# Performance work log

Hardware: AMD Instinct MI355X
Metric: run time of the kernel (lower is better)

The kernel has to match this reference:

```python
import jax, jax.numpy as jnp
import numpy as np

T = 5
EPS = 1e-05


def setup_inputs() -> dict:
    key = jax.random.key(0)
    X = jax.random.normal(key, (64, 512, 32, 32), dtype=jnp.float32)
    return {"X": X}


def reference(X):
    # IterNorm (training branch): whiten channels via Newton-Schulz inverse sqrt.
    N, C, H, W = X.shape
    x = jnp.transpose(X, (1, 0, 2, 3)).reshape(C, -1)  # [d, m], d=C, m=N*H*W
    d, m = x.shape
    mean = jnp.mean(x, axis=-1, keepdims=True)
    xc = x - mean
    I = jnp.eye(d, dtype=X.dtype)
    # Sigma = eps*I + (1/m) xc xc^T  (addmm(eps, I, 1/m, xc, xc^T))
    Sigma = EPS * I + (xc @ xc.T) / m
    rTr = 1.0 / jnp.trace(Sigma)          # (Sigma * I).sum().reciprocal()
    Sigma_N = Sigma * rTr
    P = I
    for _ in range(T):
        # P_{k+1} = 1.5*P_k - 0.5 * P_k^3 @ Sigma_N
        P = 1.5 * P - 0.5 * (P @ P @ P) @ Sigma_N
    wm = P * jnp.sqrt(rTr)                # whitening matrix ~ Sigma^{-1/2}
    xn = wm @ xc                          # [d, m]
    Xn = jnp.transpose(xn.reshape(C, N, H, W), (1, 0, 2, 3))
    return Xn
```

## Files before the change

kernel.cpp:

```cpp
#include <hip/hip_runtime.h>
#include <math.h>

#define Nn   64
#define Cc   512
#define HWs  1024
#define CHW  (Cc * HWs)
#define Mm   (Nn * HWs)
#define EPSC 1e-5f

typedef unsigned int   u32;
typedef unsigned short u16;
typedef __attribute__((ext_vector_type(8))) short  short8;
typedef __attribute__((ext_vector_type(4))) float  floatx4;

__device__ __forceinline__ u16 f2bf(float f) {
    u32 u = __float_as_uint(f);
    u += 0x7fff + ((u >> 16) & 1);
    return (u16)(u >> 16);
}
__device__ __forceinline__ float bf2f(u16 h) {
    return __uint_as_float(((u32)h) << 16);
}

__device__ __forceinline__ void gld_lds16(const u16* g, u16* l) {
    __builtin_amdgcn_global_load_lds(
        (const __attribute__((address_space(1))) u32*)g,
        (__attribute__((address_space(3))) u32*)l, 16, 0, 0);
}

__global__ __launch_bounds__(256) void convert_transpose(const float* __restrict__ X,
                                                         u16* __restrict__ Xbf,
                                                         u16* __restrict__ Xt,
                                                         float* __restrict__ meanP) {
    const int hT = blockIdx.x;
    const int h0 = hT << 6;
    const int c0 = blockIdx.y << 6;
    const int n  = blockIdx.z;
    const int t  = threadIdx.x;
    __shared__ u16   T[64][65];
    __shared__ float red[64][17];

    const float* Xn  = X   + (size_t)n * CHW;
    u16*         Xbn = Xbf + (size_t)n * CHW;
    u16*         Xtn = Xt  + (size_t)n * CHW;

    const int cl = t >> 4;
    const int h4 = (t & 15) << 2;
#pragma unroll
    for (int i = 0; i < 4; ++i) {
        const int c = cl + (i << 4);
        float4 v = *(const float4*)&Xn[(size_t)(c0 + c) * HWs + h0 + h4];
        red[c][t & 15] = v.x + v.y + v.z + v.w;
        u16 b0 = f2bf(v.x), b1 = f2bf(v.y), b2 = f2bf(v.z), b3 = f2bf(v.w);
        *(ushort4*)&Xbn[(size_t)(c0 + c) * HWs + h0 + h4] = make_ushort4(b0, b1, b2, b3);
        T[c][h4]     = b0;
        T[c][h4 + 1] = b1;
        T[c][h4 + 2] = b2;
        T[c][h4 + 3] = b3;
    }
    __syncthreads();
    const int hl = t >> 4;
    const int c4 = (t & 15) << 2;
#pragma unroll
    for (int i = 0; i < 4; ++i) {
        const int h = hl + (i << 4);
        ushort4 pk = make_ushort4(T[c4][h], T[c4 + 1][h], T[c4 + 2][h], T[c4 + 3][h]);
        *(ushort4*)&Xtn[(size_t)(h0 + h) * Cc + c0 + c4] = pk;
    }
    if (t < 64) {
        float s = 0.f;
#pragma unroll
        for (int j = 0; j < 16; ++j) s += red[t][j];
        atomicAdd(&meanP[hT * 512 + c0 + t], s);
    }
}

__global__ __launch_bounds__(256) void gram_mfma(const u16* __restrict__ Xbf,
                                                 float* __restrict__ G) {
    static const int TI[10] = {0,0,0,0,1,1,1,2,2,3};
    static const int TJ[10] = {0,1,2,3,1,2,3,2,3,3};
    const int id = blockIdx.x;
    const int q  = id >> 3;
    const int x  = q % 10;
    const int y  = (id & 7) + ((q / 10) << 3);
    const int i0 = TI[x] << 7;
    const int j0 = TJ[x] << 7;
    const int n0 = y << 1;
    const int t  = threadIdx.x;
    const int w  = t >> 6, l = t & 63;

    __shared__ u16 As[128 * 32];
    __shared__ u16 Bs[128 * 32];

    floatx4 acc[4][4];
#pragma unroll
    for (int mi = 0; mi < 4; ++mi)
#pragma unroll
        for (int ni = 0; ni < 4; ++ni) acc[mi][ni] = (floatx4){0.f, 0.f, 0.f, 0.f};

    const int lr = l >> 2;
    const int lc = (l & 3) << 3;
    const int wm = w >> 1, wn = w & 1;
    const int fm = l & 15, fq = l >> 4;

    for (int n = n0; n < n0 + 2; ++n) {
        const u16* Xn = Xbf + (size_t)n * CHW;
        for (int hw = 0; hw < HWs; hw += 32) {
#pragma unroll
            for (int p = 0; p < 2; ++p) {
                const int g   = w * 2 + p;
                const int row = g * 16 + lr;
                gld_lds16(Xn + (size_t)(i0 + row) * HWs + hw + lc, &As[g * 512]);
                gld_lds16(Xn + (size_t)(j0 + row) * HWs + hw + lc, &Bs[g * 512]);
            }
            __syncthreads();
            short8 a[4], b[4];
#pragma unroll
            for (int mi = 0; mi < 4; ++mi)
                a[mi] = *(const short8*)&As[(wm * 64 + mi * 16 + fm) * 32 + fq * 8];
#pragma unroll
            for (int ni = 0; ni < 4; ++ni)
                b[ni] = *(const short8*)&Bs[(wn * 64 + ni * 16 + fm) * 32 + fq * 8];
#pragma unroll
            for (int mi = 0; mi < 4; ++mi)
#pragma unroll
                for (int ni = 0; ni < 4; ++ni)
                    acc[mi][ni] = __builtin_amdgcn_mfma_f32_16x16x32_bf16(
                        a[mi], b[ni], acc[mi][ni], 0, 0, 0);
            __syncthreads();
        }
    }
#pragma unroll
    for (int mi = 0; mi < 4; ++mi)
#pragma unroll
        for (int ni = 0; ni < 4; ++ni)
#pragma unroll
            for (int r = 0; r < 4; ++r) {
                const int gi = i0 + wm * 64 + mi * 16 + fq * 4 + r;
                const int gj = j0 + wn * 64 + ni * 16 + fm;
                atomicAdd(&G[(size_t)gi * Cc + gj], acc[mi][ni][r]);
            }
}

__global__ __launch_bounds__(256) void trace_kernel(const float* __restrict__ G,
                                                    const float* __restrict__ meanP,
                                                    float* __restrict__ mean,
                                                    float* __restrict__ scal) {
    const int t = threadIdx.x;
    for (int c = t; c < Cc; c += 256) {
        float s = 0.f;
#pragma unroll
        for (int j = 0; j < 16; ++j) s += meanP[j * 512 + c];
        mean[c] = s * (1.0f / Mm);
    }
    __syncthreads();
    float s = 0.f;
    for (int i = t; i < Cc; i += 256)
        s += G[(size_t)i * Cc + i] * (1.0f / Mm) - mean[i] * mean[i];
    __shared__ float red[256];
    red[t] = s;
    __syncthreads();
    for (int o = 128; o > 0; o >>= 1) {
        if (t < o) red[t] += red[t + o];
        __syncthreads();
    }
    if (t == 0) {
        const float tr  = red[0] + (float)Cc * EPSC;
        const float rtr = 1.0f / tr;
        scal[0] = rtr;
        scal[1] = sqrtf(rtr);
    }
}

__global__ __launch_bounds__(256) void sigman_kernel(const float* __restrict__ G,
                                                     const float* __restrict__ mean,
                                                     const float* __restrict__ scal,
                                                     u16* __restrict__ Sh,
                                                     u16* __restrict__ Sl,
                                                     float* __restrict__ Pf,
                                                     u16* __restrict__ Ph,
                                                     u16* __restrict__ Pl) {
    const int e = blockIdx.x * 256 + threadIdx.x;
    const int i = e >> 9, j = e & 511;
    const float rtr = scal[0];
    const float g = (i <= j) ? G[(size_t)i * Cc + j] : G[(size_t)j * Cc + i];
    float sig = g * (1.0f / Mm) - mean[i] * mean[j];
    if (i == j) sig += EPSC;
    const float sN = sig * rtr;
    const u16 h = f2bf(sN);
    Sh[e] = h;
    Sl[e] = f2bf(sN - bf2f(h));
    const float pv = (i == j) ? 1.f : 0.f;
    Pf[e] = pv;
    Ph[e] = (i == j) ? (u16)0x3F80 : (u16)0;
    Pl[e] = 0;
}

__global__ __launch_bounds__(256) void mm512s(const u16* __restrict__ Ah,
                                              const u16* __restrict__ Al,
                                              const u16* __restrict__ Bh,
                                              const u16* __restrict__ Bl,
                                              float alpha,
                                              const float* __restrict__ D,
                                              float beta,
                                              float* __restrict__ Cf,
                                              u16* __restrict__ Ch,
                                              u16* __restrict__ Cl) {
    const int i0 = (blockIdx.x >> 3) << 6;
    const int j0 = (blockIdx.x & 7) << 6;
    const int t  = threadIdx.x;
    const int w  = t >> 6, l = t & 63;
    const int wm = w >> 1, wn = w & 1;
    const int fm = l & 15, fq = l >> 4;
    const int lr = l >> 2, lc = (l & 3) << 3;

    __shared__ u16 S4[4][64 * 32];

    const u16* src;
    int rbase;
    if (w == 0)      { src = Ah; rbase = i0; }
    else if (w == 1) { src = Al; rbase = i0; }
    else if (w == 2) { src = Bh; rbase = j0; }
    else             { src = Bl; rbase = j0; }

    floatx4 acc[2][2];
#pragma unroll
    for (int mi = 0; mi < 2; ++mi)
#pragma unroll
        for (int ni = 0; ni < 2; ++ni) acc[mi][ni] = (floatx4){0.f, 0.f, 0.f, 0.f};

    for (int k0 = 0; k0 < 512; k0 += 32) {
#pragma unroll
        for (int g = 0; g < 4; ++g)
            gld_lds16(src + (size_t)(rbase + g * 16 + lr) * 512 + k0 + lc,
                      &S4[w][g * 512]);
        __syncthreads();
        short8 ah[2], al[2], bh[2], bl[2];
#pragma unroll
        for (int mi = 0; mi < 2; ++mi) {
            const int ro = (wm * 32 + mi * 16 + fm) * 32 + fq * 8;
            ah[mi] = *(const short8*)&S4[0][ro];
            al[mi] = *(const short8*)&S4[1][ro];
        }
#pragma unroll
        for (int ni = 0; ni < 2; ++ni) {
            const int ro = (wn * 32 + ni * 16 + fm) * 32 + fq * 8;
            bh[ni] = *(const short8*)&S4[2][ro];
            bl[ni] = *(const short8*)&S4[3][ro];
        }
#pragma unroll
        for (int mi = 0; mi < 2; ++mi)
#pragma unroll
            for (int ni = 0; ni < 2; ++ni) {
                acc[mi][ni] = __builtin_amdgcn_mfma_f32_16x16x32_bf16(ah[mi], bh[ni], acc[mi][ni], 0, 0, 0);
                acc[mi][ni] = __builtin_amdgcn_mfma_f32_16x16x32_bf16(ah[mi], bl[ni], acc[mi][ni], 0, 0, 0);
                acc[mi][ni] = __builtin_amdgcn_mfma_f32_16x16x32_bf16(al[mi], bh[ni], acc[mi][ni], 0, 0, 0);
            }
        __syncthreads();
    }

#pragma unroll
    for (int mi = 0; mi < 2; ++mi)
#pragma unroll
        for (int ni = 0; ni < 2; ++ni)
#pragma unroll
            for (int r = 0; r < 4; ++r) {
                const int gi = i0 + wm * 32 + mi * 16 + fq * 4 + r;
                const int gj = j0 + wn * 32 + ni * 16 + fm;
                const size_t idx = (size_t)gi * 512 + gj;
                float v = alpha * acc[mi][ni][r];
                if (D) v += beta * D[idx];
                if (Cf) Cf[idx] = v;
                const u16 h = f2bf(v);
                Ch[idx] = h;
                Cl[idx] = f2bf(v - bf2f(h));
            }
}

__global__ __launch_bounds__(128) void wmm_kernel(const float* __restrict__ P,
                                                  const float* __restrict__ mean,
                                                  const float* __restrict__ scal,
                                                  float* __restrict__ wmm) {
    const int c = blockIdx.x, t = threadIdx.x;
    float s = 0.f;
    for (int j = t; j < Cc; j += 128) s += P[(size_t)c * Cc + j] * mean[j];
    __shared__ float red[128];
    red[t] = s;
    __syncthreads();
    for (int o = 64; o > 0; o >>= 1) {
        if (t < o) red[t] += red[t + o];
        __syncthreads();
    }
    if (t == 0) wmm[c] = red[0] * scal[1];
}

__global__ __launch_bounds__(256) void whiten_mfma(const u16* __restrict__ Xt,
                                                   const u16* __restrict__ Pbf,
                                                   const float* __restrict__ wmm,
                                                   const float* __restrict__ scal,
                                                   float* __restrict__ out) {
    const int id  = blockIdx.x;
    const int m   = (id >> 3) & 3;
    const int grp = (id & 7) + ((id >> 5) << 3);
    const int c0  = m << 7;
    const int h0  = (grp & 7) << 7;
    const int n   = grp >> 3;
    const int t   = threadIdx.x;
    const int w   = t >> 6, l = t & 63;

    __shared__ char smem[128 * 68 * 4];
    u16* As = (u16*)smem;
    u16* Bs = As + 4096;
    float* Ep = (float*)smem;

    floatx4 acc[4][4];
#pragma unroll
    for (int mi = 0; mi < 4; ++mi)
#pragma unroll
        for (int ni = 0; ni < 4; ++ni) acc[mi][ni] = (floatx4){0.f, 0.f, 0.f, 0.f};

    const int lr = l >> 2;
    const int lc = (l & 3) << 3;
    const int wm = w >> 1, wn = w & 1;
    const int fm = l & 15, fq = l >> 4;

    const u16* Xn = Xt + (size_t)n * CHW;

    for (int kk = 0; kk < Cc; kk += 32) {
#pragma unroll
        for (int p = 0; p < 2; ++p) {
            const int g   = w * 2 + p;
            const int row = g * 16 + lr;
            gld_lds16(Xn  + (size_t)(h0 + row) * Cc + kk + lc, &As[g * 512]);
            gld_lds16(Pbf + (size_t)(c0 + row) * Cc + kk + lc, &Bs[g * 512]);
        }
        __syncthreads();
        short8 a[4], b[4];
#pragma unroll
        for (int mi = 0; mi < 4; ++mi)
            a[mi] = *(const short8*)&As[(wm * 64 + mi * 16 + fm) * 32 + fq * 8];
#pragma unroll
        for (int ni = 0; ni < 4; ++ni)
            b[ni] = *(const short8*)&Bs[(wn * 64 + ni * 16 + fm) * 32 + fq * 8];
#pragma unroll
        for (int mi = 0; mi < 4; ++mi)
#pragma unroll
            for (int ni = 0; ni < 4; ++ni)
                acc[mi][ni] = __builtin_amdgcn_mfma_f32_16x16x32_bf16(
                    a[mi], b[ni], acc[mi][ni], 0, 0, 0);
        __syncthreads();
    }

    const float sr = scal[1];
    float wv[4];
#pragma unroll
    for (int ni = 0; ni < 4; ++ni) wv[ni] = wmm[c0 + wn * 64 + ni * 16 + fm];
    float* outn = out + (size_t)n * CHW;

#pragma unroll
    for (int mp = 0; mp < 2; ++mp) {
        __syncthreads();
#pragma unroll
        for (int p = 0; p < 2; ++p) {
            const int mi = mp * 2 + p;
#pragma unroll
            for (int ni = 0; ni < 4; ++ni) {
                const int row  = wn * 64 + ni * 16 + fm;
                const int slot = wm * 32 + p * 16 + fq * 4;
                floatx4 v = acc[mi][ni] * sr - wv[ni];
                *(floatx4*)&Ep[row * 68 + slot] = v;
            }
        }
        __syncthreads();
#pragma unroll
        for (int jj = 0; jj < 8; ++jj) {
            const int idx = jj * 256 + t;
            const int row = idx >> 4;
            const int s4  = (idx & 15) << 2;
            const int wmr = s4 >> 5;
            const int within = s4 & 31;
            float4 v = *(const float4*)&Ep[row * 68 + s4];
            *(float4*)&outn[(size_t)(c0 + row) * HWs + h0 + wmr * 64 + mp * 32 + within] = v;
        }
    }
}

__global__ __launch_bounds__(256) void mean_kernel(const float* __restrict__ X,
                                                   float* __restrict__ mean) {
    const int c = blockIdx.x;
    const int t = threadIdx.x;
    float s = 0.f;
    for (int n = 0; n < Nn; ++n) {
        const float4* p = (const float4*)(X + (size_t)n * CHW + (size_t)c * HWs);
        float4 v = p[t];
        s += v.x + v.y + v.z + v.w;
    }
    __shared__ float red[256];
    red[t] = s;
    __syncthreads();
    for (int o = 128; o > 0; o >>= 1) {
        if (t < o) red[t] += red[t + o];
        __syncthreads();
    }
    if (t == 0) mean[c] = red[0] * (1.0f / Mm);
}

__global__ __launch_bounds__(256) void trace_fb(const float* __restrict__ G,
                                                const float* __restrict__ mean,
                                                float* __restrict__ scal) {
    const int t = threadIdx.x;
    float s = 0.f;
    for (int i = t; i < Cc; i += 256)
        s += G[(size_t)i * Cc + i] * (1.0f / Mm) - mean[i] * mean[i];
    __shared__ float red[256];
    red[t] = s;
    __syncthreads();
    for (int o = 128; o > 0; o >>= 1) {
        if (t < o) red[t] += red[t + o];
        __syncthreads();
    }
    if (t == 0) {
        const float tr  = red[0] + (float)Cc * EPSC;
        const float rtr = 1.0f / tr;
        scal[0] = rtr;
        scal[1] = sqrtf(rtr);
    }
}

__global__ __launch_bounds__(256) void gram_kernel(const float* __restrict__ X,
                                                   float* __restrict__ G) {
    const int ti = blockIdx.x >> 3, tj = blockIdx.x & 7;
    const int i0 = ti << 6, j0 = tj << 6;
    const int n0 = blockIdx.y << 3;
    const int t  = threadIdx.x;
    const int tx = t & 15, ty = t >> 4;
    __shared__ float As[64][33];
    __shared__ float Bs[64][33];
    float acc[4][4] = {};
    const int lc = t & 31;
    const int lr0 = t >> 5;
    for (int n = n0; n < n0 + 8; ++n) {
        const float* Xn = X + (size_t)n * CHW;
        for (int hw0 = 0; hw0 < HWs; hw0 += 32) {
#pragma unroll
            for (int r = 0; r < 8; ++r) {
                const int row = lr0 + (r << 3);
                As[row][lc] = Xn[(size_t)(i0 + row) * HWs + hw0 + lc];
                Bs[row][lc] = Xn[(size_t)(j0 + row) * HWs + hw0 + lc];
            }
            __syncthreads();
#pragma unroll
            for (int k = 0; k < 32; ++k) {
                float a[4], b[4];
#pragma unroll
                for (int r = 0; r < 4; ++r) a[r] = As[(ty << 2) + r][k];
#pragma unroll
                for (int cn = 0; cn < 4; ++cn) b[cn] = Bs[(tx << 2) + cn][k];
#pragma unroll
                for (int r = 0; r < 4; ++r)
#pragma unroll
                    for (int cn = 0; cn < 4; ++cn) acc[r][cn] += a[r] * b[cn];
            }
            __syncthreads();
        }
    }
#pragma unroll
    for (int r = 0; r < 4; ++r)
#pragma unroll
        for (int cn = 0; cn < 4; ++cn)
            atomicAdd(&G[(size_t)(i0 + (ty << 2) + r) * Cc + j0 + (tx << 2) + cn],
                      acc[r][cn]);
}

__global__ __launch_bounds__(256) void sigman_full_kernel(const float* __restrict__ G,
                                                          const float* __restrict__ mean,
                                                          const float* __restrict__ scal,
                                                          float* __restrict__ S,
                                                          float* __restrict__ P) {
    const int e = blockIdx.x * 256 + threadIdx.x;
    const int i = e >> 9, j = e & 511;
    const float rtr = scal[0];
    float sig = G[e] * (1.0f / Mm) - mean[i] * mean[j];
    if (i == j) sig += EPSC;
    S[e] = sig * rtr;
    P[e] = (i == j) ? 1.f : 0.f;
}

__global__ __launch_bounds__(256) void mm512_kernel(const float* __restrict__ A,
                                                    const float* __restrict__ B,
                                                    float* __restrict__ C,
                                                    float alpha,
                                                    const float* __restrict__ D,
                                                    float beta) {
    const int ti = blockIdx.x >> 3, tj = blockIdx.x & 7;
    const int i0 = ti << 6, j0 = tj << 6;
    const int t  = threadIdx.x;
    const int tx = t & 15, ty = t >> 4;
    __shared__ float As[64][33];
    __shared__ float Bs[32][65];
    float acc[4][4] = {};
    const int lcA = t & 31, lrA = t >> 5;
    const int lcB = t & 63, lrB = t >> 6;
    for (int k0 = 0; k0 < 512; k0 += 32) {
#pragma unroll
        for (int r = 0; r < 8; ++r) {
            const int row = lrA + (r << 3);
            As[row][lcA] = A[(size_t)(i0 + row) * 512 + k0 + lcA];
        }
#pragma unroll
        for (int r = 0; r < 8; ++r) {
            const int row = lrB + (r << 2);
            Bs[row][lcB] = B[(size_t)(k0 + row) * 512 + j0 + lcB];
        }
        __syncthreads();
#pragma unroll
        for (int k = 0; k < 32; ++k) {
            float a[4], b[4];
#pragma unroll
            for (int r = 0; r < 4; ++r) a[r] = As[(ty << 2) + r][k];
#pragma unroll
            for (int cn = 0; cn < 4; ++cn) b[cn] = Bs[k][(tx << 2) + cn];
#pragma unroll
            for (int r = 0; r < 4; ++r)
#pragma unroll
                for (int cn = 0; cn < 4; ++cn) acc[r][cn] += a[r] * b[cn];
        }
        __syncthreads();
    }
#pragma unroll
    for (int r = 0; r < 4; ++r) {
        const size_t idx = (size_t)(i0 + (ty << 2) + r) * 512 + j0 + (tx << 2);
        float4 v;
        v.x = alpha * acc[r][0];
        v.y = alpha * acc[r][1];
        v.z = alpha * acc[r][2];
        v.w = alpha * acc[r][3];
        if (D) {
            const float4 d = *(const float4*)(D + idx);
            v.x += beta * d.x; v.y += beta * d.y; v.z += beta * d.z; v.w += beta * d.w;
        }
        *(float4*)(C + idx) = v;
    }
}

__global__ __launch_bounds__(256) void whiten_kernel(const float* __restrict__ X,
                                                     const float* __restrict__ P,
                                                     const float* __restrict__ wmm,
                                                     const float* __restrict__ scal,
                                                     float* __restrict__ out) {
    const int c0 = blockIdx.x << 6;
    const int h0 = blockIdx.y << 6;
    const int n  = blockIdx.z;
    const int t  = threadIdx.x;
    const int tx = t & 15, ty = t >> 4;
    __shared__ float Ps[64][33];
    __shared__ float Xs[32][65];
    float acc[4][4] = {};
    const int lcA = t & 31, lrA = t >> 5;
    const int lcB = t & 63, lrB = t >> 6;
    const float* Xn = X + (size_t)n * CHW;
    for (int k0 = 0; k0 < 512; k0 += 32) {
#pragma unroll
        for (int r = 0; r < 8; ++r) {
            const int row = lrA + (r << 3);
            Ps[row][lcA] = P[(size_t)(c0 + row) * 512 + k0 + lcA];
        }
#pragma unroll
        for (int r = 0; r < 8; ++r) {
            const int row = lrB + (r << 2);
            Xs[row][lcB] = Xn[(size_t)(k0 + row) * HWs + h0 + lcB];
        }
        __syncthreads();
#pragma unroll
        for (int k = 0; k < 32; ++k) {
            float a[4], b[4];
#pragma unroll
            for (int r = 0; r < 4; ++r) a[r] = Ps[(ty << 2) + r][k];
#pragma unroll
            for (int cn = 0; cn < 4; ++cn) b[cn] = Xs[k][(tx << 2) + cn];
#pragma unroll
            for (int r = 0; r < 4; ++r)
#pragma unroll
                for (int cn = 0; cn < 4; ++cn) acc[r][cn] += a[r] * b[cn];
        }
        __syncthreads();
    }
    const float sr = scal[1];
#pragma unroll
    for (int r = 0; r < 4; ++r) {
        const int c = c0 + (ty << 2) + r;
        const float wv = wmm[c];
        float4 v;
        v.x = sr * acc[r][0] - wv;
        v.y = sr * acc[r][1] - wv;
        v.z = sr * acc[r][2] - wv;
        v.w = sr * acc[r][3] - wv;
        *(float4*)(out + (size_t)n * CHW + (size_t)c * HWs + h0 + (tx << 2)) = v;
    }
}

extern "C" void kernel_launch(void* const* d_in, const int* in_sizes, int n_in,
                              void* d_out, int out_size, void* d_ws, size_t ws_size,
                              hipStream_t stream) {
    const float* X = (const float*)d_in[0];
    float* out     = (float*)d_out;

    const size_t NU16 = 33554432;
    const size_t NM   = 262144;
    const size_t NEED = NU16 * 2 * 2
                      + NM * 10 * 2
                      + (NM + 8192 + 512 + 512 + 16 + NM + NM) * 4;

    if (ws_size >= NEED) {
        u16* Xbf = (u16*)d_ws;
        u16* Xt  = Xbf + NU16;
        u16* Sh  = Xt  + NU16;
        u16* Sl  = Sh + NM;
        u16* Ph  = Sl + NM;
        u16* Pl  = Ph + NM;
        u16* Qh  = Pl + NM;
        u16* Ql  = Qh + NM;
        u16* T2h = Ql + NM;
        u16* T2l = T2h + NM;
        u16* T3h = T2l + NM;
        u16* T3l = T3h + NM;
        float* G     = (float*)(T3l + NM);
        float* meanP = G + NM;
        float* mean  = meanP + 8192;
        float* wmm   = mean + 512;
        float* scal  = wmm + 512;
        float* Pf    = scal + 16;
        float* Qf    = Pf + NM;

        hipMemsetAsync(G, 0, (NM + 8192) * sizeof(float), stream);
        convert_transpose<<<dim3(16, 8, 64), 256, 0, stream>>>(X, Xbf, Xt, meanP);
        gram_mfma<<<320, 256, 0, stream>>>(Xbf, G);
        trace_kernel<<<1, 256, 0, stream>>>(G, meanP, mean, scal);
        sigman_kernel<<<1024, 256, 0, stream>>>(G, mean, scal, Sh, Sl, Pf, Ph, Pl);

        for (int it = 0; it < 5; ++it) {
            mm512s<<<64, 256, 0, stream>>>(Ph, Pl, Ph, Pl, 1.f, nullptr, 0.f,
                                           nullptr, T2h, T2l);
            mm512s<<<64, 256, 0, stream>>>(T2h, T2l, Ph, Pl, 1.f, nullptr, 0.f,
                                           nullptr, T3h, T3l);
            mm512s<<<64, 256, 0, stream>>>(T3h, T3l, Sh, Sl, -0.5f, Pf, 1.5f,
                                           Qf, Qh, Ql);
            { float* tf = Pf; Pf = Qf; Qf = tf; }
            { u16* th = Ph; Ph = Qh; Qh = th; }
            { u16* tl = Pl; Pl = Ql; Ql = tl; }
        }

        wmm_kernel<<<512, 128, 0, stream>>>(Pf, mean, scal, wmm);
        whiten_mfma<<<2048, 256, 0, stream>>>(Xt, Ph, wmm, scal, out);
    } else {
        float* ws   = (float*)d_ws;
        float* mean = ws;
        float* wmm  = ws + 512;
        float* scal = ws + 1024;
        float* G    = ws + 2048;
        float* S    = G + 262144;
        float* Pa   = S + 262144;
        float* Pb   = Pa + 262144;
        float* P2   = Pb + 262144;
        float* P3   = P2 + 262144;

        mean_kernel<<<512, 256, 0, stream>>>(X, mean);
        hipMemsetAsync(G, 0, sizeof(float) * 262144, stream);
        gram_kernel<<<dim3(64, 8), 256, 0, stream>>>(X, G);
        trace_fb<<<1, 256, 0, stream>>>(G, mean, scal);
        sigman_full_kernel<<<1024, 256, 0, stream>>>(G, mean, scal, S, Pa);

        float* P  = Pa;
        float* Pn = Pb;
        for (int it = 0; it < 5; ++it) {
            mm512_kernel<<<64, 256, 0, stream>>>(P, P, P2, 1.f, nullptr, 0.f);
            mm512_kernel<<<64, 256, 0, stream>>>(P2, P, P3, 1.f, nullptr, 0.f);
            mm512_kernel<<<64, 256, 0, stream>>>(P3, S, Pn, -0.5f, P, 1.5f);
            float* tmp = P; P = Pn; Pn = tmp;
        }

        wmm_kernel<<<512, 128, 0, stream>>>(P, mean, scal, wmm);
        whiten_kernel<<<dim3(8, 16, 64), 256, 0, stream>>>(X, P, wmm, scal, out);
    }
}
```

Measured before the change: 549.7 us.

## Fuse Newton-Schulz chain into one persistent kernel with grid barriers

```diff
diff --git a/kernel.cpp b/kernel.cpp
--- a/kernel.cpp
+++ b/kernel.cpp
@@ -7,6 +7,7 @@
 #define CHW  (Cc * HWs)
 #define Mm   (Nn * HWs)
 #define EPSC 1e-5f
+#define NBC  64
 
 typedef unsigned int   u32;
 typedef unsigned short u16;
@@ -142,86 +143,31 @@
             }
 }
 
-__global__ __launch_bounds__(256) void trace_kernel(const float* __restrict__ G,
-                                                    const float* __restrict__ meanP,
-                                                    float* __restrict__ mean,
-                                                    float* __restrict__ scal) {
-    const int t = threadIdx.x;
-    for (int c = t; c < Cc; c += 256) {
-        float s = 0.f;
-#pragma unroll
-        for (int j = 0; j < 16; ++j) s += meanP[j * 512 + c];
-        mean[c] = s * (1.0f / Mm);
-    }
+__device__ __forceinline__ void gridbar(int* bar, int gen) {
     __syncthreads();
-    float s = 0.f;
-    for (int i = t; i < Cc; i += 256)
-        s += G[(size_t)i * Cc + i] * (1.0f / Mm) - mean[i] * mean[i];
-    __shared__ float red[256];
-    red[t] = s;
+    if (threadIdx.x == 0) {
+        __threadfence();
+        __hip_atomic_fetch_add(bar, 1, __ATOMIC_RELEASE, __HIP_MEMORY_SCOPE_AGENT);
+        while (__hip_atomic_load(bar, __ATOMIC_ACQUIRE, __HIP_MEMORY_SCOPE_AGENT) < gen * NBC)
+            __builtin_amdgcn_s_sleep(1);
+        __threadfence();
+    }
     __syncthreads();
-    for (int o = 128; o > 0; o >>= 1) {
-        if (t < o) red[t] += red[t + o];
-        __syncthreads();
-    }
-    if (t == 0) {
-        const float tr  = red[0] + (float)Cc * EPSC;
-        const float rtr = 1.0f / tr;
-        scal[0] = rtr;
-        scal[1] = sqrtf(rtr);
-    }
-}
-
-__global__ __launch_bounds__(256) void sigman_kernel(const float* __restrict__ G,
-                                                     const float* __restrict__ mean,
-                                                     const float* __restrict__ scal,
-                                                     u16* __restrict__ Sh,
-                                                     u16* __restrict__ Sl,
-                                                     float* __restrict__ Pf,
-                                                     u16* __restrict__ Ph,
-                                                     u16* __restrict__ Pl) {
-    const int e = blockIdx.x * 256 + threadIdx.x;
-    const int i = e >> 9, j = e & 511;
-    const float rtr = scal[0];
-    const float g = (i <= j) ? G[(size_t)i * Cc + j] : G[(size_t)j * Cc + i];
-    float sig = g * (1.0f / Mm) - mean[i] * mean[j];
-    if (i == j) sig += EPSC;
-    const float sN = sig * rtr;
-    const u16 h = f2bf(sN);
-    Sh[e] = h;
-    Sl[e] = f2bf(sN - bf2f(h));
-    const float pv = (i == j) ? 1.f : 0.f;
-    Pf[e] = pv;
-    Ph[e] = (i == j) ? (u16)0x3F80 : (u16)0;
-    Pl[e] = 0;
-}
-
-__global__ __launch_bounds__(256) void mm512s(const u16* __restrict__ Ah,
-                                              const u16* __restrict__ Al,
-                                              const u16* __restrict__ Bh,
-                                              const u16* __restrict__ Bl,
-                                              float alpha,
-                                              const float* __restrict__ D,
-                                              float beta,
-                                              float* __restrict__ Cf,
-                                              u16* __restrict__ Ch,
-                                              u16* __restrict__ Cl) {
-    const int i0 = (blockIdx.x >> 3) << 6;
-    const int j0 = (blockIdx.x & 7) << 6;
-    const int t  = threadIdx.x;
-    const int w  = t >> 6, l = t & 63;
-    const int wm = w >> 1, wn = w & 1;
-    const int fm = l & 15, fq = l >> 4;
-    const int lr = l >> 2, lc = (l & 3) << 3;
-
-    __shared__ u16 S4[4][64 * 32];
-
-    const u16* src;
-    int rbase;
-    if (w == 0)      { src = Ah; rbase = i0; }
-    else if (w == 1) { src = Al; rbase = i0; }
-    else if (w == 2) { src = Bh; rbase = j0; }
-    else             { src = Bl; rbase = j0; }
+}
+
+__device__ void mm_phase(const u16* Ah, const u16* Al, const u16* Bh, const u16* Bl,
+                         float alpha, const float* D, float beta,
+                         float* Cf, u16* Ch, u16* Cl, u16* S) {
+    const int bid = blockIdx.x;
+    const int i0 = (bid >> 3) << 6, j0 = (bid & 7) << 6;
+    const int t = threadIdx.x, w = t >> 6, l = t & 63;
+    const int wm = w >> 1, wn = w & 1, fm = l & 15, fq = l >> 4;
+    const u16* src = (w == 0) ? Ah : (w == 1) ? Al : (w == 2) ? Bh : Bl;
+    const int rbase = (w < 2) ? i0 : j0;
+    u16* myl = S + (w << 12);
+    const int srow = l >> 3;
+    const int skb  = ((l & 7) ^ srow) << 3;
+    const int f7   = fm & 7;
 
     floatx4 acc[2][2];
 #pragma unroll
@@ -229,33 +175,39 @@
 #pragma unroll
         for (int ni = 0; ni < 2; ++ni) acc[mi][ni] = (floatx4){0.f, 0.f, 0.f, 0.f};
 
-    for (int k0 = 0; k0 < 512; k0 += 32) {
-#pragma unroll
-        for (int g = 0; g < 4; ++g)
-            gld_lds16(src + (size_t)(rbase + g * 16 + lr) * 512 + k0 + lc,
-                      &S4[w][g * 512]);
-        __syncthreads();
-        short8 ah[2], al[2], bh[2], bl[2];
-#pragma unroll
-        for (int mi = 0; mi < 2; ++mi) {
-            const int ro = (wm * 32 + mi * 16 + fm) * 32 + fq * 8;
-            ah[mi] = *(const short8*)&S4[0][ro];
-            al[mi] = *(const short8*)&S4[1][ro];
-        }
-#pragma unroll
-        for (int ni = 0; ni < 2; ++ni) {
-            const int ro = (wn * 32 + ni * 16 + fm) * 32 + fq * 8;
-            bh[ni] = *(const short8*)&S4[2][ro];
-            bl[ni] = *(const short8*)&S4[3][ro];
-        }
-#pragma unroll
-        for (int mi = 0; mi < 2; ++mi)
+    for (int k0 = 0; k0 < 512; k0 += 64) {
+#pragma unroll
+        for (int g = 0; g < 8; ++g)
+            gld_lds16(src + (size_t)(rbase + (g << 3) + srow) * 512 + k0 + skb,
+                      myl + (g << 9));
+        __syncthreads();
+#pragma unroll
+        for (int kc = 0; kc < 2; ++kc) {
+            short8 ah[2], al[2], bh[2], bl[2];
+            const int kq = ((kc << 2) + fq);
+#pragma unroll
+            for (int mi = 0; mi < 2; ++mi) {
+                const int r   = wm * 32 + mi * 16 + fm;
+                const int off = (r << 6) + ((kq ^ f7) << 3);
+                ah[mi] = *(const short8*)&S[off];
+                al[mi] = *(const short8*)&S[4096 + off];
+            }
 #pragma unroll
             for (int ni = 0; ni < 2; ++ni) {
-                acc[mi][ni] = __builtin_amdgcn_mfma_f32_16x16x32_bf16(ah[mi], bh[ni], acc[mi][ni], 0, 0, 0);
-                acc[mi][ni] = __builtin_amdgcn_mfma_f32_16x16x32_bf16(ah[mi], bl[ni], acc[mi][ni], 0, 0, 0);
-                acc[mi][ni] = __builtin_amdgcn_mfma_f32_16x16x32_bf16(al[mi], bh[ni], acc[mi][ni], 0, 0, 0);
+                const int r   = wn * 32 + ni * 16 + fm;
+                const int off = (r << 6) + ((kq ^ f7) << 3);
+                bh[ni] = *(const short8*)&S[8192 + off];
+                bl[ni] = *(const short8*)&S[12288 + off];
             }
+#pragma unroll
+            for (int mi = 0; mi < 2; ++mi)
+#pragma unroll
+                for (int ni = 0; ni < 2; ++ni) {
+                    acc[mi][ni] = __builtin_amdgcn_mfma_f32_16x16x32_bf16(ah[mi], bh[ni], acc[mi][ni], 0, 0, 0);
+                    acc[mi][ni] = __builtin_amdgcn_mfma_f32_16x16x32_bf16(ah[mi], bl[ni], acc[mi][ni], 0, 0, 0);
+                    acc[mi][ni] = __builtin_amdgcn_mfma_f32_16x16x32_bf16(al[mi], bh[ni], acc[mi][ni], 0, 0, 0);
+                }
+        }
         __syncthreads();
     }
 
@@ -264,11 +216,11 @@
 #pragma unroll
         for (int ni = 0; ni < 2; ++ni)
 #pragma unroll
-            for (int r = 0; r < 4; ++r) {
-                const int gi = i0 + wm * 32 + mi * 16 + fq * 4 + r;
+            for (int r4 = 0; r4 < 4; ++r4) {
+                const int gi = i0 + wm * 32 + mi * 16 + fq * 4 + r4;
                 const int gj = j0 + wn * 32 + ni * 16 + fm;
                 const size_t idx = (size_t)gi * 512 + gj;
-                float v = alpha * acc[mi][ni][r];
+                float v = alpha * acc[mi][ni][r4];
                 if (D) v += beta * D[idx];
                 if (Cf) Cf[idx] = v;
                 const u16 h = f2bf(v);
@@ -277,21 +229,86 @@
             }
 }
 
-__global__ __launch_bounds__(128) void wmm_kernel(const float* __restrict__ P,
-                                                  const float* __restrict__ mean,
-                                                  const float* __restrict__ scal,
-                                                  float* __restrict__ wmm) {
-    const int c = blockIdx.x, t = threadIdx.x;
-    float s = 0.f;
-    for (int j = t; j < Cc; j += 128) s += P[(size_t)c * Cc + j] * mean[j];
-    __shared__ float red[128];
-    red[t] = s;
-    __syncthreads();
-    for (int o = 64; o > 0; o >>= 1) {
-        if (t < o) red[t] += red[t + o];
-        __syncthreads();
-    }
-    if (t == 0) wmm[c] = red[0] * scal[1];
+__global__ __launch_bounds__(256) void ns_chain(
+    const float* G, const float* meanP, float* scal, int* bar,
+    float* mean, float* wmmv,
+    u16* Sh, u16* Sl, u16* PhA, u16* PlA, u16* PhB, u16* PlB,
+    u16* T2h, u16* T2l, u16* T3h, u16* T3l, float* PfA, float* PfB) {
+    __shared__ u16 S[4 * 4096];
+    const int t = threadIdx.x, b = blockIdx.x;
+
+    {
+        const int c = b * 8 + (t >> 5);
+        const int q = t & 31;
+        float s = (q < 16) ? meanP[(size_t)q * 512 + c] : 0.f;
+#pragma unroll
+        for (int o = 16; o > 0; o >>= 1) s += __shfl_xor(s, o);
+        if (q == 0) {
+            const float mc = s * (1.0f / Mm);
+            mean[c] = mc;
+            const float tc = G[(size_t)c * 513] * (1.0f / Mm) - mc * mc;
+            atomicAdd(&scal[2], tc);
+        }
+    }
+    gridbar(bar, 1);
+    if (b == 0 && t == 0) {
+        const float tr  = scal[2] + (float)Cc * EPSC;
+        const float rtr = 1.0f / tr;
+        scal[0] = rtr;
+        scal[1] = sqrtf(rtr);
+    }
+    gridbar(bar, 2);
+
+    {
+        const float rtr = scal[0];
+#pragma unroll
+        for (int k2 = 0; k2 < 16; ++k2) {
+            const int e = (b << 12) + (k2 << 8) + t;
+            const int i = e >> 9, j = e & 511;
+            const float g = (i <= j) ? G[((size_t)i << 9) + j] : G[((size_t)j << 9) + i];
+            float sig = g * (1.0f / Mm) - mean[i] * mean[j];
+            if (i == j) sig += EPSC;
+            const float sN = sig * rtr;
+            const u16 sh = f2bf(sN);
+            Sh[e] = sh;
+            Sl[e] = f2bf(sN - bf2f(sh));
+            const float p1 = ((i == j) ? 1.5f : 0.f) - 0.5f * sN;
+            PfA[e] = p1;
+            const u16 ph = f2bf(p1);
+            PhA[e] = ph;
+            PlA[e] = f2bf(p1 - bf2f(ph));
+        }
+    }
+    gridbar(bar, 3);
+
+    int gen = 3;
+    u16 *ph = PhA, *pl = PlA, *qh = PhB, *ql = PlB;
+    float *pf = PfA, *qf = PfB;
+    for (int it = 0; it < 4; ++it) {
+        mm_phase(ph, pl, ph, pl, 1.f, nullptr, 0.f, nullptr, T2h, T2l, S);
+        gridbar(bar, ++gen);
+        mm_phase(T2h, T2l, ph, pl, 1.f, nullptr, 0.f, nullptr, T3h, T3l, S);
+        gridbar(bar, ++gen);
+        mm_phase(T3h, T3l, Sh, Sl, -0.5f, pf, 1.5f, qf, qh, ql, S);
+        gridbar(bar, ++gen);
+        { u16* x = ph; ph = qh; qh = x; }
+        { u16* x = pl; pl = ql; ql = x; }
+        { float* x = pf; pf = qf; qf = x; }
+    }
+
+    {
+        const int c = b * 8 + (t >> 5);
+        const int q = t & 31;
+        float s = 0.f;
+#pragma unroll
+        for (int k2 = 0; k2 < 16; ++k2) {
+            const int j = q + (k2 << 5);
+            s += pf[((size_t)c << 9) + j] * mean[j];
+        }
+#pragma unroll
+        for (int o = 16; o > 0; o >>= 1) s += __shfl_xor(s, o);
+        if (q == 0) wmmv[c] = s * scal[1];
+    }
 }
 
 __global__ __launch_bounds__(256) void whiten_mfma(const u16* __restrict__ Xt,
@@ -541,6 +558,23 @@
         }
         *(float4*)(C + idx) = v;
     }
+}
+
+__global__ __launch_bounds__(128) void wmm_kernel(const float* __restrict__ P,
+                                                  const float* __restrict__ mean,
+                                                  const float* __restrict__ scal,
+                                                  float* __restrict__ wmm) {
+    const int c = blockIdx.x, t = threadIdx.x;
+    float s = 0.f;
+    for (int j = t; j < Cc; j += 128) s += P[(size_t)c * Cc + j] * mean[j];
+    __shared__ float red[128];
+    red[t] = s;
+    __syncthreads();
+    for (int o = 64; o > 0; o >>= 1) {
+        if (t < o) red[t] += red[t + o];
+        __syncthreads();
+    }
+    if (t == 0) wmm[c] = red[0] * scal[1];
 }
 
 __global__ __launch_bounds__(256) void whiten_kernel(const float* __restrict__ X,
@@ -609,49 +643,37 @@
     const size_t NM   = 262144;
     const size_t NEED = NU16 * 2 * 2
                       + NM * 10 * 2
-                      + (NM + 8192 + 512 + 512 + 16 + NM + NM) * 4;
+                      + (NM + 8192 + 32 + 512 + 512 + 2 * NM) * 4;
 
     if (ws_size >= NEED) {
         u16* Xbf = (u16*)d_ws;
         u16* Xt  = Xbf + NU16;
         u16* Sh  = Xt  + NU16;
         u16* Sl  = Sh + NM;
-        u16* Ph  = Sl + NM;
-        u16* Pl  = Ph + NM;
-        u16* Qh  = Pl + NM;
-        u16* Ql  = Qh + NM;
-        u16* T2h = Ql + NM;
+        u16* PhA = Sl + NM;
+        u16* PlA = PhA + NM;
+        u16* PhB = PlA + NM;
+        u16* PlB = PhB + NM;
+        u16* T2h = PlB + NM;
         u16* T2l = T2h + NM;
         u16* T3h = T2l + NM;
         u16* T3l = T3h + NM;
         float* G     = (float*)(T3l + NM);
         float* meanP = G + NM;
-        float* mean  = meanP + 8192;
+        float* scal  = meanP + 8192;
+        int*   bar   = (int*)(scal + 16);
+        float* mean  = (float*)(bar + 16);
         float* wmm   = mean + 512;
-        float* scal  = wmm + 512;
-        float* Pf    = scal + 16;
-        float* Qf    = Pf + NM;
-
-        hipMemsetAsync(G, 0, (NM + 8192) * sizeof(float), stream);
+        float* PfA   = wmm + 512;
+        float* PfB   = PfA + NM;
+
+        hipMemsetAsync(G, 0, (NM + 8192 + 32) * sizeof(float), stream);
         convert_transpose<<<dim3(16, 8, 64), 256, 0, stream>>>(X, Xbf, Xt, meanP);
         gram_mfma<<<320, 256, 0, stream>>>(Xbf, G);
-        trace_kernel<<<1, 256, 0, stream>>>(G, meanP, mean, scal);
-        sigman_kernel<<<1024, 256, 0, stream>>>(G, mean, scal, Sh, Sl, Pf, Ph, Pl);
-
-        for (int it = 0; it < 5; ++it) {
-            mm512s<<<64, 256, 0, stream>>>(Ph, Pl, Ph, Pl, 1.f, nullptr, 0.f,
-                                           nullptr, T2h, T2l);
-            mm512s<<<64, 256, 0, stream>>>(T2h, T2l, Ph, Pl, 1.f, nullptr, 0.f,
-                                           nullptr, T3h, T3l);
-            mm512s<<<64, 256, 0, stream>>>(T3h, T3l, Sh, Sl, -0.5f, Pf, 1.5f,
-                                           Qf, Qh, Ql);
-            { float* tf = Pf; Pf = Qf; Qf = tf; }
-            { u16* th = Ph; Ph = Qh; Qh = th; }
-            { u16* tl = Pl; Pl = Ql; Ql = tl; }
-        }
-
-        wmm_kernel<<<512, 128, 0, stream>>>(Pf, mean, scal, wmm);
-        whiten_mfma<<<2048, 256, 0, stream>>>(Xt, Ph, wmm, scal, out);
+        ns_chain<<<NBC, 256, 0, stream>>>(G, meanP, scal, bar, mean, wmm,
+                                          Sh, Sl, PhA, PlA, PhB, PlB,
+                                          T2h, T2l, T3h, T3l, PfA, PfB);
+        whiten_mfma<<<2048, 256, 0, stream>>>(Xt, PhA, wmm, scal, out);
     } else {
         float* ws   = (float*)d_ws;
         float* mean = ws;
```

New measurement: 547.8 us. About the same (-0.4%).
